# Kernel tuning notes

Measured on AMD Instinct MI355X. Metric: run time of the kernel, lower is better.

Reference implementation:

```python
import jax, jax.numpy as jnp
import numpy as np

N_NODES = 100000
N_EDGES = 1600000
NFEAT, NHID, NCLASS = 256, 128, 40


def setup_inputs() -> dict:
    key = jax.random.key(0)
    ks = jax.random.split(key, 10)
    x = jax.random.normal(ks[0], (N_NODES, NFEAT), dtype=jnp.float32)
    edge_row = jnp.sort(jax.random.randint(ks[1], (N_EDGES,), 0, N_NODES, dtype=jnp.int64))
    edge_col = jax.random.randint(ks[2], (N_EDGES,), 0, N_NODES, dtype=jnp.int64)
    edge_val = jax.random.uniform(ks[3], (N_EDGES,), dtype=jnp.float32)
    s = 0.05  # small init scale for numerical stability
    w1 = jax.random.normal(ks[4], (NFEAT, NHID), dtype=jnp.float32) * s
    b1 = jax.random.normal(ks[5], (NHID,), dtype=jnp.float32) * s
    w2 = jax.random.normal(ks[6], (NHID, NHID // 2), dtype=jnp.float32) * s
    b2 = jax.random.normal(ks[7], (NHID // 2,), dtype=jnp.float32) * s
    wl = jax.random.normal(ks[8], (NHID + NHID // 2, NCLASS), dtype=jnp.float32) * s
    bl = jax.random.normal(ks[9], (NCLASS,), dtype=jnp.float32) * s
    return {"x": x, "edge_row": edge_row, "edge_col": edge_col, "edge_val": edge_val,
            "w1": w1, "b1": b1, "w2": w2, "b2": b2, "wl": wl, "bl": bl}


def _gcn_layer(h, w, b, edge_row, edge_col, edge_val, n_nodes):
    # support = h @ W; out = spmm(adj, support) + b  (pygcn GraphConvolution)
    support = h @ w                                   # [N, d_out]
    msg = support[edge_col] * edge_val[:, None]       # gather src + edge weight, [E, d_out]
    agg = jax.ops.segment_sum(msg, edge_row, num_segments=n_nodes)  # scatter-add to dst
    return agg + b


def reference(x, edge_row, edge_col, edge_val, w1, b1, w2, b2, wl, bl):
    n = x.shape[0]
    x1 = jax.nn.relu(_gcn_layer(x, w1, b1, edge_row, edge_col, edge_val, n))
    # dropout is identity in eval mode
    x2 = jax.nn.relu(_gcn_layer(x1, w2, b2, edge_row, edge_col, edge_val, n))
    out = jnp.concatenate([x2, x1], axis=1) @ wl + bl
    return jax.nn.log_softmax(out, axis=-1)
```

## Files before the change

kernel.cpp:

```cpp
#include <hip/hip_runtime.h>
#include <math.h>

#define N_NODES 100000
#define N_EDGES 1600000
#define NFEAT   256
#define NHID    128
#define NHID2   64
#define NCLASS  40
#define NCLS_P  64

typedef __attribute__((ext_vector_type(8))) short bf16x8;
typedef __attribute__((ext_vector_type(4))) float f32x4;
typedef __attribute__((ext_vector_type(2))) float f32x2;

static __device__ inline unsigned short f2bf(float f) {
    union { float f; unsigned u; } v; v.f = f;
    unsigned r = v.u + 0x7FFF + ((v.u >> 16) & 1);
    return (unsigned short)(r >> 16);
}
static __device__ inline unsigned pkbf(float a, float b) {
    return (unsigned)f2bf(a) | ((unsigned)f2bf(b) << 16);
}
static __device__ inline float bfl(unsigned u) {
    union { unsigned u; float f; } v; v.u = u << 16; return v.f;
}
static __device__ inline float bfraw(unsigned u) {
    union { unsigned u; float f; } v; v.u = u; return v.f;
}

#if __has_builtin(__builtin_amdgcn_cvt_pk_fp8_f32) && __has_builtin(__builtin_amdgcn_cvt_pk_f32_fp8)
#define FP8_HW 1
#else
#define FP8_HW 0
static __device__ inline unsigned f2fp8_sw(float f) {
    union { float f; unsigned u; } v; v.f = f;
    unsigned s = (v.u >> 24) & 0x80u;
    int e = (int)((v.u >> 23) & 0xFF) - 120;
    unsigned m = v.u & 0x7FFFFFu;
    if (e < 1) return s;
    unsigned keep = m >> 20, rest = m & 0xFFFFFu;
    keep += (rest > 0x80000u) || (rest == 0x80000u && (keep & 1));
    if (keep == 8) { keep = 0; ++e; }
    if (e > 15) { e = 15; keep = 6; }
    return s | ((unsigned)e << 3) | keep;
}
static __device__ inline float fp8f_sw(unsigned b) {
    unsigned e = (b >> 3) & 0xF;
    union { unsigned u; float f; } v;
    v.u = ((b & 0x80u) << 24) | ((e + 120) << 23) | ((b & 7u) << 20);
    return e ? v.f : 0.f;
}
#endif

static __device__ inline unsigned pack4_fp8(float a, float b, float c, float d) {
#if FP8_HW
    int r = __builtin_amdgcn_cvt_pk_fp8_f32(a, b, 0, false);
    r = __builtin_amdgcn_cvt_pk_fp8_f32(c, d, r, true);
    return (unsigned)r;
#else
    return f2fp8_sw(a) | (f2fp8_sw(b) << 8) | (f2fp8_sw(c) << 16) | (f2fp8_sw(d) << 24);
#endif
}
static __device__ inline void unpack4_fp8(unsigned g, f32x2& lo, f32x2& hi) {
#if FP8_HW
    lo = __builtin_amdgcn_cvt_pk_f32_fp8((int)g, false);
    hi = __builtin_amdgcn_cvt_pk_f32_fp8((int)g, true);
#else
    lo.x = fp8f_sw(g & 0xFF); lo.y = fp8f_sw((g >> 8) & 0xFF);
    hi.x = fp8f_sw((g >> 16) & 0xFF); hi.y = fp8f_sw(g >> 24);
#endif
}

#define PREP_T0 (N_NODES + 1)
#define PREP_T1 (PREP_T0 + NHID * NFEAT)
#define PREP_T2 (PREP_T1 + NHID2 * NHID)
#define PREP_T3 (PREP_T2 + NCLS_P * 192)
#define PREP_T4 (PREP_T3 + N_EDGES)
__global__ void prep(const int* __restrict__ er, int* __restrict__ row_ptr,
                     const float* __restrict__ w1, unsigned short* __restrict__ w1t,
                     const float* __restrict__ w2, unsigned short* __restrict__ w2t,
                     const float* __restrict__ wl, unsigned short* __restrict__ wlt,
                     const int* __restrict__ ec, const float* __restrict__ ev,
                     uint2* __restrict__ meta) {
    int idx = blockIdx.x * blockDim.x + threadIdx.x;
    if (idx < PREP_T0) {
        int lo = 0, hi = N_EDGES;
        while (lo < hi) { int mid = (lo + hi) >> 1; if (er[mid] < idx) lo = mid + 1; else hi = mid; }
        row_ptr[idx] = lo;
    } else if (idx < PREP_T1) {
        int i = idx - PREP_T0;
        int n = i >> 8, k = i & 255;
        w1t[i] = f2bf(w1[k * NHID + n]);
    } else if (idx < PREP_T2) {
        int i = idx - PREP_T1;
        int n = i >> 7, k = i & 127;
        w2t[i] = f2bf(w2[k * NHID2 + n]);
    } else if (idx < PREP_T3) {
        int i = idx - PREP_T2;
        int n = i / 192, k = i - n * 192;
        wlt[i] = (n < NCLASS) ? f2bf(wl[k * NCLASS + n]) : (unsigned short)0;
    } else if (idx < PREP_T4) {
        int i = idx - PREP_T3;
        uint2 m; m.x = (unsigned)ec[i];
        union { float f; unsigned u; } v; v.f = ev[i];
        m.y = v.u;
        meta[i] = m;
    }
}

__global__ __launch_bounds__(512) void gemm1_full(const float* __restrict__ A,
                                                  const unsigned short* __restrict__ Bt,
                                                  unsigned char* __restrict__ C, int M) {
    const int K = 256, S = K + 8;
    extern __shared__ char smem[];
    unsigned short* As = (unsigned short*)smem;
    unsigned short* Bs = As + 128 * S;

    int tid = threadIdx.x;
    int lane = tid & 63, wid = tid >> 6;
    int wr = wid >> 2, wc = wid & 3;
    int row0 = blockIdx.x * 128;

    #pragma unroll
    for (int ch = 0; ch < 4; ++ch) {
        float4 av[4];
        #pragma unroll
        for (int i = 0; i < 4; ++i) {
            int s = tid + (ch * 4 + i) * 512;
            int m = s >> 6, c = (s & 63) * 4;
            int row = row0 + m;
            av[i] = (row < M) ? *(const float4*)(A + (size_t)row * K + c)
                              : float4{0.f, 0.f, 0.f, 0.f};
        }
        #pragma unroll
        for (int i = 0; i < 4; ++i) {
            int s = tid + (ch * 4 + i) * 512;
            int m = s >> 6, c = (s & 63) * 4;
            uint2 p; p.x = pkbf(av[i].x, av[i].y); p.y = pkbf(av[i].z, av[i].w);
            *(uint2*)&As[m * S + c] = p;
        }
    }
    #pragma unroll
    for (int ch = 0; ch < 2; ++ch) {
        uint4 bv[4];
        #pragma unroll
        for (int i = 0; i < 4; ++i) {
            int s = tid + (ch * 4 + i) * 512;
            int n = s >> 5, kk = (s & 31) * 8;
            bv[i] = *(const uint4*)(Bt + (size_t)n * K + kk);
        }
        #pragma unroll
        for (int i = 0; i < 4; ++i) {
            int s = tid + (ch * 4 + i) * 512;
            int n = s >> 5, kk = (s & 31) * 8;
            *(uint4*)&Bs[n * S + kk] = bv[i];
        }
    }
    __syncthreads();

    f32x4 acc[4][2];
    #pragma unroll
    for (int i = 0; i < 4; ++i)
        #pragma unroll
        for (int j = 0; j < 2; ++j) acc[i][j] = f32x4{0.f, 0.f, 0.f, 0.f};

    #pragma unroll
    for (int t = 0; t < 8; ++t) {
        bf16x8 af[4], bfr[2];
        #pragma unroll
        for (int mi = 0; mi < 4; ++mi)
            af[mi] = *(const bf16x8*)&As[(wr * 64 + mi * 16 + (lane & 15)) * S + t * 32 + ((lane >> 4) << 3)];
        #pragma unroll
        for (int ni = 0; ni < 2; ++ni)
            bfr[ni] = *(const bf16x8*)&Bs[(wc * 32 + ni * 16 + (lane & 15)) * S + t * 32 + ((lane >> 4) << 3)];
        #pragma unroll
        for (int mi = 0; mi < 4; ++mi)
            #pragma unroll
            for (int ni = 0; ni < 2; ++ni)
                acc[mi][ni] = __builtin_amdgcn_mfma_f32_16x16x32_bf16(af[mi], bfr[ni], acc[mi][ni], 0, 0, 0);
    }

    __syncthreads();
    float* Lf = (float*)As; const int LS = 132;
    #pragma unroll
    for (int mi = 0; mi < 4; ++mi) {
        int rt = wr * 64 + mi * 16 + ((lane >> 4) << 2);
        #pragma unroll
        for (int ni = 0; ni < 2; ++ni) {
            int ct = wc * 32 + ni * 16 + (lane & 15);
            #pragma unroll
            for (int r = 0; r < 4; ++r) Lf[(rt + r) * LS + ct] = acc[mi][ni][r];
        }
    }
    __syncthreads();
    int rl = tid >> 2, c0 = (tid & 3) * 32;
    int row = row0 + rl;
    if (row < M) {
        unsigned u[8];
        #pragma unroll
        for (int q = 0; q < 8; ++q) {
            f32x4 v = *(const f32x4*)&Lf[rl * LS + c0 + q * 4];
            u[q] = pack4_fp8(v[0], v[1], v[2], v[3]);
        }
        unsigned char* o = C + (size_t)row * 128 + c0;
        *(uint4*)o = uint4{u[0], u[1], u[2], u[3]};
        *(uint4*)(o + 16) = uint4{u[4], u[5], u[6], u[7]};
    }
}

template <int BN, int K>
__global__ __launch_bounds__(512) void gemm_full(const unsigned short* __restrict__ A,
                                                 const unsigned short* __restrict__ Bt,
                                                 unsigned short* __restrict__ C,
                                                 int M, int lda, int ldc) {
    const int S   = K + 8;
    const int OCT = K / 8;
    const int WC  = (BN == 128) ? 4 : 2;
    const int MF  = (BN == 128) ? 4 : 2;
    const int NF  = 2;
    const int NT  = K / 32;

    extern __shared__ char smem[];
    unsigned short* As = (unsigned short*)smem;
    unsigned short* Bs = As + 128 * S;

    int tid = threadIdx.x;
    int lane = tid & 63, wid = tid >> 6;
    int wr = wid / WC, wc = wid % WC;
    int row0 = blockIdx.x * 128;

    {
        const int NI = 128 * OCT / 512;
        uint4 av[NI];
        #pragma unroll
        for (int i = 0; i < NI; ++i) {
            int s = tid + i * 512;
            int m = s / OCT, kk = (s - m * OCT) * 8;
            int row = row0 + m;
            av[i] = (row < M) ? *(const uint4*)(A + (size_t)row * lda + kk)
                              : uint4{0u, 0u, 0u, 0u};
        }
        #pragma unroll
        for (int i = 0; i < NI; ++i) {
            int s = tid + i * 512;
            int m = s / OCT, kk = (s - m * OCT) * 8;
            *(uint4*)&As[m * S + kk] = av[i];
        }
    }
    {
        const int NI = BN * OCT / 512;
        uint4 bv[NI];
        #pragma unroll
        for (int i = 0; i < NI; ++i) {
            int s = tid + i * 512;
            int n = s / OCT, kk = (s - n * OCT) * 8;
            bv[i] = *(const uint4*)(Bt + (size_t)n * K + kk);
        }
        #pragma unroll
        for (int i = 0; i < NI; ++i) {
            int s = tid + i * 512;
            int n = s / OCT, kk = (s - n * OCT) * 8;
            *(uint4*)&Bs[n * S + kk] = bv[i];
        }
    }
    __syncthreads();

    f32x4 acc[MF][NF];
    #pragma unroll
    for (int i = 0; i < MF; ++i)
        #pragma unroll
        for (int j = 0; j < NF; ++j) acc[i][j] = f32x4{0.f, 0.f, 0.f, 0.f};

    #pragma unroll
    for (int t = 0; t < NT; ++t) {
        bf16x8 af[MF], bfr[NF];
        #pragma unroll
        for (int mi = 0; mi < MF; ++mi)
            af[mi] = *(const bf16x8*)&As[(wr * (MF * 16) + mi * 16 + (lane & 15)) * S + t * 32 + (lane >> 4) * 8];
        #pragma unroll
        for (int ni = 0; ni < NF; ++ni)
            bfr[ni] = *(const bf16x8*)&Bs[(wc * (NF * 16) + ni * 16 + (lane & 15)) * S + t * 32 + (lane >> 4) * 8];
        #pragma unroll
        for (int mi = 0; mi < MF; ++mi)
            #pragma unroll
            for (int ni = 0; ni < NF; ++ni)
                acc[mi][ni] = __builtin_amdgcn_mfma_f32_16x16x32_bf16(af[mi], bfr[ni], acc[mi][ni], 0, 0, 0);
    }

    #pragma unroll
    for (int mi = 0; mi < MF; ++mi) {
        int rbase = row0 + wr * (MF * 16) + mi * 16 + ((lane >> 4) << 2);
        #pragma unroll
        for (int ni = 0; ni < NF; ++ni) {
            int col = wc * (NF * 16) + ni * 16 + (lane & 15);
            #pragma unroll
            for (int r = 0; r < 4; ++r) {
                int row = rbase + r;
                if (row < M) C[(size_t)row * ldc + col] = f2bf(acc[mi][ni][r]);
            }
        }
    }
}

__global__ __launch_bounds__(256) void spmm_fp8(const unsigned char* __restrict__ sup8,
                                                const int* __restrict__ row_ptr,
                                                const uint2* __restrict__ meta,
                                                const float* __restrict__ bias,
                                                unsigned short* __restrict__ out,
                                                int out_stride, int n_nodes) {
    __shared__ uint2 mlds[4][64];

    int wave = threadIdx.x >> 6;
    int lane = threadIdx.x & 63;
    int node = blockIdx.x * 4 + wave;
    if (node >= n_nodes) return;

    int sub = lane >> 5, l = lane & 31;
    int e0 = row_ptr[node];
    int cnt = row_ptr[node + 1] - e0;
    unsigned loff = (unsigned)(l << 2);

    f32x2 a0 = {0.f, 0.f}, a1 = {0.f, 0.f};

    for (int o = 0; o < cnt; o += 64) {
        int rem = min(64, cnt - o);
        uint2 m;
        if (lane < rem) m = meta[e0 + o + lane];
        else { m.x = 0u; m.y = 0u; }
        mlds[wave][lane] = m;

        for (int j = 0; j < rem; j += 16) {
            unsigned g[8]; float vv[8];
            #pragma unroll
            for (int t = 0; t < 8; ++t) {
                uint2 cm = mlds[wave][j + 2 * t + sub];
                g[t] = *(const unsigned*)(sup8 + (((size_t)cm.x) << 7) + loff);
                union { unsigned u; float f; } c; c.u = cm.y;
                vv[t] = c.f;
            }
            #pragma unroll
            for (int t = 0; t < 8; ++t) {
                f32x2 lo, hi;
                unpack4_fp8(g[t], lo, hi);
                f32x2 v2 = {vv[t], vv[t]};
                a0 += v2 * lo;
                a1 += v2 * hi;
            }
        }
    }

    a0.x += __shfl_xor(a0.x, 32); a0.y += __shfl_xor(a0.y, 32);
    a1.x += __shfl_xor(a1.x, 32); a1.y += __shfl_xor(a1.y, 32);

    if (lane < 32) {
        float4 bv = *(const float4*)(bias + 4 * l);
        float r0 = a0.x + bv.x, r1 = a0.y + bv.y;
        float r2 = a1.x + bv.z, r3 = a1.y + bv.w;
        r0 = r0 > 0.f ? r0 : 0.f; r1 = r1 > 0.f ? r1 : 0.f;
        r2 = r2 > 0.f ? r2 : 0.f; r3 = r3 > 0.f ? r3 : 0.f;
        uint2 pk; pk.x = pkbf(r0, r1); pk.y = pkbf(r2, r3);
        *(uint2*)(out + (size_t)node * out_stride + 4 * l) = pk;
    }
}

__global__ __launch_bounds__(256) void spmm_bf16_64(const unsigned short* __restrict__ sup,
                                                    const int* __restrict__ row_ptr,
                                                    const uint2* __restrict__ meta,
                                                    const float* __restrict__ bias,
                                                    unsigned short* __restrict__ out,
                                                    int out_stride, int n_nodes) {
    __shared__ uint2 mlds[4][64];

    int wave = threadIdx.x >> 6;
    int lane = threadIdx.x & 63;
    int node = blockIdx.x * 4 + wave;
    if (node >= n_nodes) return;

    int sub = lane >> 4, l = lane & 15;
    int e0 = row_ptr[node];
    int cnt = row_ptr[node + 1] - e0;
    const char* base = (const char*)sup;
    unsigned loff = (unsigned)(l << 3);

    f32x2 a0 = {0.f, 0.f}, a1 = {0.f, 0.f};

    for (int o = 0; o < cnt; o += 64) {
        int rem = min(64, cnt - o);
        uint2 m;
        if (lane < rem) m = meta[e0 + o + lane];
        else { m.x = 0u; m.y = 0u; }
        mlds[wave][lane] = m;

        for (int j = 0; j < rem; j += 32) {
            uint2 g[8]; float vv[8];
            #pragma unroll
            for (int t = 0; t < 8; ++t) {
                uint2 cm = mlds[wave][j + 4 * t + sub];
                unsigned voff = (cm.x << 7) + loff;
                g[t] = *(const uint2*)(base + voff);
                union { unsigned u; float f; } c; c.u = cm.y;
                vv[t] = c.f;
            }
            #pragma unroll
            for (int t = 0; t < 8; ++t) {
                f32x2 v2 = {vv[t], vv[t]};
                f32x2 f0 = {bfl(g[t].x), bfraw(g[t].x)};
                f32x2 f1 = {bfl(g[t].y), bfraw(g[t].y)};
                a0 += v2 * f0;
                a1 += v2 * f1;
            }
        }
    }

    a0.x += __shfl_xor(a0.x, 32); a0.y += __shfl_xor(a0.y, 32);
    a1.x += __shfl_xor(a1.x, 32); a1.y += __shfl_xor(a1.y, 32);
    a0.x += __shfl_xor(a0.x, 16); a0.y += __shfl_xor(a0.y, 16);
    a1.x += __shfl_xor(a1.x, 16); a1.y += __shfl_xor(a1.y, 16);

    if (lane < 16) {
        float4 bv = *(const float4*)(bias + 4 * l);
        float r0 = a0.x + bv.x, r1 = a0.y + bv.y;
        float r2 = a1.x + bv.z, r3 = a1.y + bv.w;
        r0 = r0 > 0.f ? r0 : 0.f; r1 = r1 > 0.f ? r1 : 0.f;
        r2 = r2 > 0.f ? r2 : 0.f; r3 = r3 > 0.f ? r3 : 0.f;
        uint2 pk; pk.x = pkbf(r0, r1); pk.y = pkbf(r2, r3);
        *(uint2*)(out + (size_t)node * out_stride + 4 * l) = pk;
    }
}

__global__ __launch_bounds__(512) void head_fused(const unsigned short* __restrict__ A,
                                                  const unsigned short* __restrict__ Bt,
                                                  const float* __restrict__ bl,
                                                  float* __restrict__ out, int M) {
    const int K = 192, S = K + 8, OCT = K / 8;
    const int MF = 2, NF = 2, NT = 6;

    extern __shared__ char smem[];
    unsigned short* As = (unsigned short*)smem;
    unsigned short* Bs = As + 128 * S;
    float* L  = (float*)(Bs + 64 * S);
    float* bls = L + 128 * 65;

    int tid = threadIdx.x;
    int lane = tid & 63, wid = tid >> 6;
    int wr = wid >> 1, wc = wid & 1;
    int row0 = blockIdx.x * 128;
    if (tid < NCLASS) bls[tid] = bl[tid];

    {
        uint4 av[6];
        #pragma unroll
        for (int i = 0; i < 6; ++i) {
            int s = tid + i * 512;
            int m = s / OCT, kk = (s - m * OCT) * 8;
            int row = row0 + m;
            av[i] = (row < M) ? *(const uint4*)(A + (size_t)row * 192 + kk)
                              : uint4{0u, 0u, 0u, 0u};
        }
        #pragma unroll
        for (int i = 0; i < 6; ++i) {
            int s = tid + i * 512;
            int m = s / OCT, kk = (s - m * OCT) * 8;
            *(uint4*)&As[m * S + kk] = av[i];
        }
    }
    {
        uint4 bv[3];
        #pragma unroll
        for (int i = 0; i < 3; ++i) {
            int s = tid + i * 512;
            int n = s / OCT, kk = (s - n * OCT) * 8;
            bv[i] = *(const uint4*)(Bt + (size_t)n * 192 + kk);
        }
        #pragma unroll
        for (int i = 0; i < 3; ++i) {
            int s = tid + i * 512;
            int n = s / OCT, kk = (s - n * OCT) * 8;
            *(uint4*)&Bs[n * S + kk] = bv[i];
        }
    }
    __syncthreads();

    f32x4 acc[MF][NF];
    #pragma unroll
    for (int i = 0; i < MF; ++i)
        #pragma unroll
        for (int j = 0; j < NF; ++j) acc[i][j] = f32x4{0.f, 0.f, 0.f, 0.f};

    #pragma unroll
    for (int t = 0; t < NT; ++t) {
        bf16x8 af[MF], bfr[NF];
        #pragma unroll
        for (int mi = 0; mi < MF; ++mi)
            af[mi] = *(const bf16x8*)&As[(wr * 32 + mi * 16 + (lane & 15)) * S + t * 32 + (lane >> 4) * 8];
        #pragma unroll
        for (int ni = 0; ni < NF; ++ni)
            bfr[ni] = *(const bf16x8*)&Bs[(wc * 32 + ni * 16 + (lane & 15)) * S + t * 32 + (lane >> 4) * 8];
        #pragma unroll
        for (int mi = 0; mi < MF; ++mi)
            #pragma unroll
            for (int ni = 0; ni < NF; ++ni)
                acc[mi][ni] = __builtin_amdgcn_mfma_f32_16x16x32_bf16(af[mi], bfr[ni], acc[mi][ni], 0, 0, 0);
    }

    #pragma unroll
    for (int mi = 0; mi < MF; ++mi) {
        int rt = wr * 32 + mi * 16 + ((lane >> 4) << 2);
        #pragma unroll
        for (int ni = 0; ni < NF; ++ni) {
            int ct = wc * 32 + ni * 16 + (lane & 15);
            #pragma unroll
            for (int r = 0; r < 4; ++r) L[(rt + r) * 65 + ct] = acc[mi][ni][r];
        }
    }
    __syncthreads();

    {
        int r = tid >> 2, h = tid & 3;
        int row = row0 + r;
        if (row < M) {
            float vals[10];
            float m = -1e30f;
            #pragma unroll
            for (int c = 0; c < 10; ++c) {
                float tv = L[r * 65 + h * 10 + c] + bls[h * 10 + c];
                vals[c] = tv;
                m = fmaxf(m, tv);
            }
            m = fmaxf(m, __shfl_xor(m, 1));
            m = fmaxf(m, __shfl_xor(m, 2));
            float s = 0.f;
            #pragma unroll
            for (int c = 0; c < 10; ++c) s += __expf(vals[c] - m);
            s += __shfl_xor(s, 1);
            s += __shfl_xor(s, 2);
            float lg = __logf(s);
            float* o = out + (size_t)row * NCLASS + h * 10;
            #pragma unroll
            for (int c = 0; c < 10; ++c) o[c] = vals[c] - m - lg;
        }
    }
}

extern "C" void kernel_launch(void* const* d_in, const int* in_sizes, int n_in,
                              void* d_out, int out_size, void* d_ws, size_t ws_size,
                              hipStream_t stream) {
    const float* x        = (const float*)d_in[0];
    const int*   edge_row = (const int*)d_in[1];
    const int*   edge_col = (const int*)d_in[2];
    const float* edge_val = (const float*)d_in[3];
    const float* w1       = (const float*)d_in[4];
    const float* b1       = (const float*)d_in[5];
    const float* w2       = (const float*)d_in[6];
    const float* b2       = (const float*)d_in[7];
    const float* wl       = (const float*)d_in[8];
    const float* bl       = (const float*)d_in[9];
    float* out = (float*)d_out;
    (void)in_sizes; (void)n_in; (void)out_size; (void)ws_size;

    char* ws = (char*)d_ws;
    size_t off = 0;
    int* row_ptr = (int*)(ws + off);
    off += (((size_t)(N_NODES + 1) * sizeof(int)) + 255) & ~(size_t)255;
    unsigned short* x_cat = (unsigned short*)(ws + off);
    off += (size_t)N_NODES * 192 * sizeof(short);
    unsigned short* sup = (unsigned short*)(ws + off);
    off += (size_t)N_NODES * NHID * sizeof(short);
    unsigned char* sup8 = (unsigned char*)(ws + off);
    off += (size_t)N_NODES * NHID;
    uint2* meta = (uint2*)(ws + off);   off += (size_t)N_EDGES * sizeof(uint2);
    unsigned short* w1t = (unsigned short*)(ws + off); off += (size_t)NHID * NFEAT * sizeof(short);
    unsigned short* w2t = (unsigned short*)(ws + off); off += (size_t)NHID2 * NHID * sizeof(short);
    unsigned short* wlt = (unsigned short*)(ws + off); off += (size_t)NCLS_P * 192 * sizeof(short);

    unsigned short* x1 = x_cat + NHID2;
    unsigned short* x2 = x_cat;

    prep<<<(PREP_T4 + 255) / 256, 256, 0, stream>>>(edge_row, row_ptr, w1, w1t, w2, w2t, wl, wlt,
                                                    edge_col, edge_val, meta);

    int mblocks = (N_NODES + 127) / 128;

    const int smem1 = (128 + 128) * (NFEAT + 8) * 2;
    const int smem2 = (128 + 64) * (NHID + 8) * 2;
    const int smemH = (128 + 64) * (192 + 8) * 2 + 128 * 65 * 4 + NCLASS * 4;

    gemm1_full<<<dim3(mblocks, 1), 512, smem1, stream>>>(x, w1t, sup8, N_NODES);
    spmm_fp8<<<(N_NODES + 3) / 4, 256, 0, stream>>>(sup8, row_ptr, meta, b1, x1, 192, N_NODES);

    gemm_full<NHID2, NHID><<<dim3(mblocks, 1), 512, smem2, stream>>>(x1, w2t, sup, N_NODES, 192, NHID2);
    spmm_bf16_64<<<(N_NODES + 3) / 4, 256, 0, stream>>>(sup, row_ptr, meta, b2, x2, 192, N_NODES);

    head_fused<<<dim3(mblocks, 1), 512, smemH, stream>>>(x_cat, wlt, bl, out, N_NODES);
}
```

Measured before the change: 151.2 us.

## Keep W1 fragments in registers and shrink gemm1 tile to 64 rows

The first GEMM kernel no longer stages the transposed W1 in shared memory. Each wave now loads its 32-column slice of W1 straight from global memory into registers as MFMA B fragments. The block tile shrinks from 128 to 64 rows with 256 threads, and launch bounds request 4 blocks per CU. This cuts LDS use per block and removes the B-tile LDS reads, to raise occupancy and better hide the latency of streaming the fp32 input. In exchange it adds register pressure from 64 VGPRs of B fragments, and each block re-reads W1 from L2.

```diff
diff --git a/kernel.cpp b/kernel.cpp
--- a/kernel.cpp
+++ b/kernel.cpp
@@ -108,25 +108,32 @@
     }
 }
 
-__global__ __launch_bounds__(512) void gemm1_full(const float* __restrict__ A,
-                                                  const unsigned short* __restrict__ Bt,
-                                                  unsigned char* __restrict__ C, int M) {
+__global__ __launch_bounds__(256, 4) void gemm1_breg(const float* __restrict__ A,
+                                                     const unsigned short* __restrict__ Bt,
+                                                     unsigned char* __restrict__ C, int M) {
     const int K = 256, S = K + 8;
     extern __shared__ char smem[];
     unsigned short* As = (unsigned short*)smem;
-    unsigned short* Bs = As + 128 * S;
 
     int tid = threadIdx.x;
-    int lane = tid & 63, wid = tid >> 6;
-    int wr = wid >> 2, wc = wid & 3;
-    int row0 = blockIdx.x * 128;
+    int lane = tid & 63, wc = tid >> 6;
+    int row0 = blockIdx.x * 64;
+
+    bf16x8 br[2][8];
+    #pragma unroll
+    for (int ni = 0; ni < 2; ++ni)
+        #pragma unroll
+        for (int t = 0; t < 8; ++t) {
+            int n = wc * 32 + ni * 16 + (lane & 15);
+            br[ni][t] = *(const bf16x8*)(Bt + (size_t)n * K + t * 32 + ((lane >> 4) << 3));
+        }
 
     #pragma unroll
     for (int ch = 0; ch < 4; ++ch) {
         float4 av[4];
         #pragma unroll
         for (int i = 0; i < 4; ++i) {
-            int s = tid + (ch * 4 + i) * 512;
+            int s = tid + (ch * 4 + i) * 256;
             int m = s >> 6, c = (s & 63) * 4;
             int row = row0 + m;
             av[i] = (row < M) ? *(const float4*)(A + (size_t)row * K + c)
@@ -134,28 +141,12 @@
         }
         #pragma unroll
         for (int i = 0; i < 4; ++i) {
-            int s = tid + (ch * 4 + i) * 512;
+            int s = tid + (ch * 4 + i) * 256;
             int m = s >> 6, c = (s & 63) * 4;
             uint2 p; p.x = pkbf(av[i].x, av[i].y); p.y = pkbf(av[i].z, av[i].w);
             *(uint2*)&As[m * S + c] = p;
         }
     }
-    #pragma unroll
-    for (int ch = 0; ch < 2; ++ch) {
-        uint4 bv[4];
-        #pragma unroll
-        for (int i = 0; i < 4; ++i) {
-            int s = tid + (ch * 4 + i) * 512;
-            int n = s >> 5, kk = (s & 31) * 8;
-            bv[i] = *(const uint4*)(Bt + (size_t)n * K + kk);
-        }
-        #pragma unroll
-        for (int i = 0; i < 4; ++i) {
-            int s = tid + (ch * 4 + i) * 512;
-            int n = s >> 5, kk = (s & 31) * 8;
-            *(uint4*)&Bs[n * S + kk] = bv[i];
-        }
-    }
     __syncthreads();
 
     f32x4 acc[4][2];
@@ -166,25 +157,22 @@
 
     #pragma unroll
     for (int t = 0; t < 8; ++t) {
-        bf16x8 af[4], bfr[2];
+        bf16x8 af[4];
         #pragma unroll
         for (int mi = 0; mi < 4; ++mi)
-            af[mi] = *(const bf16x8*)&As[(wr * 64 + mi * 16 + (lane & 15)) * S + t * 32 + ((lane >> 4) << 3)];
-        #pragma unroll
-        for (int ni = 0; ni < 2; ++ni)
-            bfr[ni] = *(const bf16x8*)&Bs[(wc * 32 + ni * 16 + (lane & 15)) * S + t * 32 + ((lane >> 4) << 3)];
+            af[mi] = *(const bf16x8*)&As[(mi * 16 + (lane & 15)) * S + t * 32 + ((lane >> 4) << 3)];
         #pragma unroll
         for (int mi = 0; mi < 4; ++mi)
             #pragma unroll
             for (int ni = 0; ni < 2; ++ni)
-                acc[mi][ni] = __builtin_amdgcn_mfma_f32_16x16x32_bf16(af[mi], bfr[ni], acc[mi][ni], 0, 0, 0);
+                acc[mi][ni] = __builtin_amdgcn_mfma_f32_16x16x32_bf16(af[mi], br[ni][t], acc[mi][ni], 0, 0, 0);
     }
 
     __syncthreads();
     float* Lf = (float*)As; const int LS = 132;
     #pragma unroll
     for (int mi = 0; mi < 4; ++mi) {
-        int rt = wr * 64 + mi * 16 + ((lane >> 4) << 2);
+        int rt = mi * 16 + ((lane >> 4) << 2);
         #pragma unroll
         for (int ni = 0; ni < 2; ++ni) {
             int ct = wc * 32 + ni * 16 + (lane & 15);
@@ -579,17 +567,15 @@
     prep<<<(PREP_T4 + 255) / 256, 256, 0, stream>>>(edge_row, row_ptr, w1, w1t, w2, w2t, wl, wlt,
                                                     edge_col, edge_val, meta);
 
-    int mblocks = (N_NODES + 127) / 128;
-
-    const int smem1 = (128 + 128) * (NFEAT + 8) * 2;
+    const int smem1 = 64 * (NFEAT + 8) * 2;
     const int smem2 = (128 + 64) * (NHID + 8) * 2;
     const int smemH = (128 + 64) * (192 + 8) * 2 + 128 * 65 * 4 + NCLASS * 4;
 
-    gemm1_full<<<dim3(mblocks, 1), 512, smem1, stream>>>(x, w1t, sup8, N_NODES);
+    gemm1_breg<<<dim3((N_NODES + 63) / 64, 1), 256, smem1, stream>>>(x, w1t, sup8, N_NODES);
     spmm_fp8<<<(N_NODES + 3) / 4, 256, 0, stream>>>(sup8, row_ptr, meta, b1, x1, 192, N_NODES);
 
-    gemm_full<NHID2, NHID><<<dim3(mblocks, 1), 512, smem2, stream>>>(x1, w2t, sup, N_NODES, 192, NHID2);
+    gemm_full<NHID2, NHID><<<dim3((N_NODES + 127) / 128, 1), 512, smem2, stream>>>(x1, w2t, sup, N_NODES, 192, NHID2);
     spmm_bf16_64<<<(N_NODES + 3) / 4, 256, 0, stream>>>(sup, row_ptr, meta, b2, x2, 192, N_NODES);
 
-    head_fused<<<dim3(mblocks, 1), 512, smemH, stream>>>(x_cat, wlt, bl, out, N_NODES);
-}
+    head_fused<<<dim3((N_NODES + 127) / 128, 1), 512, smemH, stream>>>(x_cat, wlt, bl, out, N_NODES);
+}
```

Result: faster. 143.9 us (-4.8%).
